# Kernel optimization log

Hardware: AMD Instinct MI355X
Metric: run time of the kernel (lower is better)

Reference implementation:

```python
import jax, jax.numpy as jnp
import numpy as np
from jax import lax

NUM_QUBITS = 4
NUM_LAYERS = 2
EPS = 1e-5  # BatchNorm eps; eval mode with running_mean=0, running_var=1


def _cnot_ring_matrix():
    # CNOT(0,1); CNOT(1,2); CNOT(2,3); CNOT(3,0) as one 16x16 permutation.
    # PennyLane convention: wire 0 is the most-significant bit of the basis index.
    M = np.zeros((16, 16), dtype=np.complex64)
    for b in range(16):
        bb = b
        for cw, tw in [(0, 1), (1, 2), (2, 3), (3, 0)]:
            if (bb >> (3 - cw)) & 1:
                bb ^= 1 << (3 - tw)
        M[bb, b] = 1.0
    return M

CNOT_RING = jnp.asarray(_cnot_ring_matrix())
# ZSIGNS[w, b] = <b|Z_w|b> = +/-1
ZSIGNS = jnp.asarray(np.array([[1.0 - 2.0 * ((b >> (3 - w)) & 1) for b in range(16)]
                               for w in range(NUM_QUBITS)], dtype=np.float32))


def conv_bn_relu(x, w, b, gamma, beta):
    # Conv2d(k=3, pad=1) + BatchNorm2d (eval: mean=0, var=1) + ReLU, NCHW
    x = lax.conv_general_dilated(x, w, (1, 1), ((1, 1), (1, 1)),
                                 dimension_numbers=('NCHW', 'OIHW', 'NCHW'))
    x = x + b[None, :, None, None]
    x = gamma[None, :, None, None] * x * (1.0 / np.sqrt(1.0 + EPS)) + beta[None, :, None, None]
    return jax.nn.relu(x)


def maxpool2(x):
    return lax.reduce_window(x, -jnp.inf, lax.max, (1, 1, 2, 2), (1, 1, 2, 2), 'VALID')


def avgpool2(x):
    return lax.reduce_window(x, 0.0, lax.add, (1, 1, 2, 2), (1, 1, 2, 2), 'VALID') * 0.25


def quantum_layer(x, weights):
    # x: [B, 16] softmax outputs. Amplitude-encode (abs + L2 normalize), then
    # BasicEntanglerLayers (RX rotations + CNOT ring) x NUM_LAYERS, then <Z_i>.
    psi = jnp.abs(x)
    psi = psi / jnp.linalg.norm(psi, axis=1, keepdims=True)
    psi = psi.astype(jnp.complex64)  # [B, 16] batched statevectors
    for l in range(NUM_LAYERS):
        c = jnp.cos(weights[l] * 0.5).astype(jnp.complex64)
        s = jnp.sin(weights[l] * 0.5).astype(jnp.complex64)
        U = jnp.ones((1, 1), dtype=jnp.complex64)
        for q in range(NUM_QUBITS):
            g = jnp.stack([jnp.stack([c[q], -1j * s[q]]),
                           jnp.stack([-1j * s[q], c[q]])])  # RX(theta_q)
            U = jnp.kron(U, g)
        U = CNOT_RING @ U  # rotations first, then entangling ring
        psi = psi @ U.T    # batched apply: [B,16] x [16,16]
    probs = jnp.real(psi * jnp.conj(psi))  # [B, 16]
    return probs @ ZSIGNS.T                # [B, 4] Pauli-Z expvals


def setup_inputs() -> dict:
    key = jax.random.key(0)
    ks = jax.random.split(key, 16)
    B = 1024
    f32 = jnp.float32

    def w(k, shape, fan_in):
        return jax.random.normal(k, shape, dtype=f32) * np.float32(1.0 / np.sqrt(fan_in))

    inp = {
        'x': jax.random.normal(ks[0], (B, 3, 32, 32), dtype=f32),
        'conv1_w': w(ks[1], (32, 3, 3, 3), 3 * 9), 'conv1_b': jnp.zeros((32,), f32),
        'bn1_g': jnp.ones((32,), f32), 'bn1_b': jnp.zeros((32,), f32),
        'conv2_w': w(ks[2], (64, 32, 3, 3), 32 * 9), 'conv2_b': jnp.zeros((64,), f32),
        'bn2_g': jnp.ones((64,), f32), 'bn2_b': jnp.zeros((64,), f32),
        'conv3_w': w(ks[3], (128, 64, 3, 3), 64 * 9), 'conv3_b': jnp.zeros((128,), f32),
        'bn3_g': jnp.ones((128,), f32), 'bn3_b': jnp.zeros((128,), f32),
        'fr1_w': w(ks[4], (512, 2048), 2048), 'fr1_b': jnp.zeros((512,), f32),
        'fr2_w': w(ks[5], (16, 512), 512), 'fr2_b': jnp.zeros((16,), f32),
        'q_weights': jax.random.uniform(ks[6], (NUM_LAYERS, NUM_QUBITS), dtype=f32,
                                        minval=0.0, maxval=2.0 * np.pi),
        'h1_w': w(ks[7], (128, 4), 4), 'h1_b': jnp.zeros((128,), f32),
        'bnh_g': jnp.ones((128,), f32), 'bnh_b': jnp.zeros((128,), f32),
        'h2_w': w(ks[8], (100, 128), 128), 'h2_b': jnp.zeros((100,), f32),
    }
    return inp


def reference(x, conv1_w, conv1_b, bn1_g, bn1_b, conv2_w, conv2_b, bn2_g, bn2_b,
              conv3_w, conv3_b, bn3_g, bn3_b, fr1_w, fr1_b, fr2_w, fr2_b,
              q_weights, h1_w, h1_b, bnh_g, bnh_b, h2_w, h2_b):
    # classical_net (CIFAR100 branch)
    h = conv_bn_relu(x, conv1_w, conv1_b, bn1_g, bn1_b)
    h = maxpool2(h)                                   # [B,32,16,16]
    h = conv_bn_relu(h, conv2_w, conv2_b, bn2_g, bn2_b)
    h = maxpool2(h)                                   # [B,64,8,8]
    h = conv_bn_relu(h, conv3_w, conv3_b, bn3_g, bn3_b)  # [B,128,8,8]
    h = avgpool2(h)                                   # AdaptiveAvgPool2d((4,4)): 8->4
    h = h.reshape(h.shape[0], -1)                     # [B, 2048]
    # feature_reducer
    h = jax.nn.relu(h @ fr1_w.T + fr1_b)
    f = jax.nn.softmax(h @ fr2_w.T + fr2_b, axis=1)   # [B, 16]
    # quantum layer (batched 4-qubit statevector sim)
    q = quantum_layer(f, q_weights)                   # [B, 4]
    # head (BN eval-mode, Dropout inactive)
    y = q @ h1_w.T + h1_b
    y = bnh_g * y * (1.0 / np.sqrt(1.0 + EPS)) + bnh_b
    y = jax.nn.relu(y)
    return y @ h2_w.T + h2_b                          # [B, 100]
```

## Files before the change

kernel.cpp:

```cpp
#include <hip/hip_runtime.h>
#include <math.h>

#define NB 1024
static constexpr float BN_INV = 0.99999500003749975f;

typedef __attribute__((ext_vector_type(8))) short short8;
typedef __attribute__((ext_vector_type(4))) float f32x4;

__device__ inline short f2bf(float f) {
  union { float f; unsigned u; } v;
  v.f = f;
  unsigned u = v.u;
  u += 0x7fff + ((u >> 16) & 1);
  return (short)(u >> 16);
}

__global__ void k_prepack(const float* __restrict__ c2w, const float* __restrict__ c2b,
                          const float* __restrict__ g2, const float* __restrict__ be2,
                          const float* __restrict__ c3w, const float* __restrict__ c3b,
                          const float* __restrict__ g3, const float* __restrict__ be3,
                          const float* __restrict__ fr1w,
                          short* __restrict__ wp2, short* __restrict__ wp3,
                          float* __restrict__ scsh, short* __restrict__ wfr1) {
  int i = blockIdx.x * 256 + threadIdx.x;
  int stride = gridDim.x * 256;
  for (int e = i; e < 18432; e += stride) {
    int j = e & 7, lane = (e >> 3) & 63, ct = (e >> 9) & 3, off = e >> 11;
    int co = ct * 16 + (lane & 15), ci = (lane >> 4) * 8 + j;
    wp2[e] = f2bf(c2w[(co * 32 + ci) * 9 + off]);
  }
  for (int e = i; e < 73728; e += stride) {
    int j = e & 7, lane = (e >> 3) & 63, ct = (e >> 9) & 7, oh = e >> 12;
    int half = oh & 1, off = oh >> 1;
    int co = ct * 16 + (lane & 15), ci = half * 32 + (lane >> 4) * 8 + j;
    wp3[e] = f2bf(c3w[(co * 64 + ci) * 9 + off]);
  }
  for (int e = i; e < 524288; e += stride) {
    float2 f = ((const float2*)fr1w)[e];
    unsigned lo = (unsigned)(unsigned short)f2bf(f.x);
    unsigned hi = (unsigned)(unsigned short)f2bf(f.y);
    ((unsigned*)wfr1)[e] = (hi << 16) | lo;
  }
  if (i < 64) {
    float sc = g2[i] * BN_INV;
    scsh[i] = sc;
    scsh[64 + i] = sc * c2b[i] + be2[i];
  } else if (i < 192) {
    int c = i - 64;
    float sc = g3[c] * BN_INV;
    scsh[128 + c] = sc;
    scsh[256 + c] = sc * c3b[c] + be3[c];
  }
}

__global__ __launch_bounds__(256) void k_conv1(
    const float* __restrict__ x, const float* __restrict__ w,
    const float* __restrict__ bias, const float* __restrict__ g,
    const float* __restrict__ be, short* __restrict__ out) {
  __shared__ float tile[3 * 34 * 34];
  const int b = blockIdx.x;
  const int tid = threadIdx.x;
  const float* xb = x + b * 3 * 32 * 32;
  for (int i = tid; i < 3 * 34 * 34; i += 256) {
    int c = i / 1156;
    int rem = i - c * 1156;
    int r = rem / 34;
    int col = rem - r * 34;
    int iy = r - 1, ix = col - 1;
    float v = 0.f;
    if (iy >= 0 && iy < 32 && ix >= 0 && ix < 32)
      v = xb[(c * 32 + iy) * 32 + ix];
    tile[i] = v;
  }
  __syncthreads();
  const int tx = tid & 15, ty = tid >> 4;
  float win[3][4][4];
#pragma unroll
  for (int c = 0; c < 3; ++c)
#pragma unroll
    for (int r = 0; r < 4; ++r)
#pragma unroll
      for (int cc = 0; cc < 4; ++cc)
        win[c][r][cc] = tile[c * 1156 + (2 * ty + r) * 34 + 2 * tx + cc];

  for (int co = 0; co < 32; ++co) {
    const float* wp = w + co * 27;
    float a00 = 0.f, a01 = 0.f, a10 = 0.f, a11 = 0.f;
#pragma unroll
    for (int c = 0; c < 3; ++c)
#pragma unroll
      for (int ky = 0; ky < 3; ++ky)
#pragma unroll
        for (int kx = 0; kx < 3; ++kx) {
          float wv = wp[c * 9 + ky * 3 + kx];
          a00 = fmaf(win[c][ky][kx], wv, a00);
          a01 = fmaf(win[c][ky][kx + 1], wv, a01);
          a10 = fmaf(win[c][ky + 1][kx], wv, a10);
          a11 = fmaf(win[c][ky + 1][kx + 1], wv, a11);
        }
    float gg = g[co] * BN_INV, bt = be[co], bs = bias[co];
    float v0 = fmaxf(fmaf(gg, a00 + bs, bt), 0.f);
    float v1 = fmaxf(fmaf(gg, a01 + bs, bt), 0.f);
    float v2 = fmaxf(fmaf(gg, a10 + bs, bt), 0.f);
    float v3 = fmaxf(fmaf(gg, a11 + bs, bt), 0.f);
    float m = fmaxf(fmaxf(v0, v1), fmaxf(v2, v3));
    out[((b * 32 + co) * 16 + ty) * 16 + tx] = f2bf(m);
  }
}

__global__ __launch_bounds__(256) void k_conv2m(
    const short* __restrict__ in ,
    const short* __restrict__ wp2, const float* __restrict__ scsh,
    short* __restrict__ out2 ) {
  __shared__ __align__(16) short inT[18 * 18 * 40];
  const int b = blockIdx.x;
  const int tid = threadIdx.x;
  const int w = tid >> 6, lane = tid & 63, q = lane >> 4, n = lane & 15;

  for (int i = tid; i < 18 * 18 * 40 / 2; i += 256) ((int*)inT)[i] = 0;
  __syncthreads();
  const short* ib = in + (size_t)b * 8192;
  for (int i = tid; i < 8192; i += 256) {
    int ci = i >> 8, y = (i >> 4) & 15, x = i & 15;
    inT[((y + 1) * 18 + (x + 1)) * 40 + ci] = ib[i];
  }
  __syncthreads();

  const short8* wv = (const short8*)wp2;
  f32x4 acc[4][4];
#pragma unroll
  for (int t = 0; t < 4; ++t)
#pragma unroll
    for (int ct = 0; ct < 4; ++ct) acc[t][ct] = (f32x4)0.f;

#pragma unroll
  for (int off = 0; off < 9; ++off) {
    const int ky = off / 3, kx = off % 3;
    short8 a[4];
#pragma unroll
    for (int ct = 0; ct < 4; ++ct) a[ct] = wv[(off * 4 + ct) * 64 + lane];
#pragma unroll
    for (int t = 0; t < 4; ++t) {
      int y = 4 * w + t;
      short8 bf = *(const short8*)&inT[((y + ky) * 18 + (n + kx)) * 40 + q * 8];
#pragma unroll
      for (int ct = 0; ct < 4; ++ct)
        acc[t][ct] =
            __builtin_amdgcn_mfma_f32_16x16x32_bf16(a[ct], bf, acc[t][ct], 0, 0, 0);
    }
  }

  const float* sc2 = scsh;
  const float* sh2 = scsh + 64;
#pragma unroll
  for (int ct = 0; ct < 4; ++ct) {
    float vm[4][4];
#pragma unroll
    for (int t = 0; t < 4; ++t)
#pragma unroll
      for (int r = 0; r < 4; ++r) {
        int co = ct * 16 + q * 4 + r;
        float v = fmaf(sc2[co], acc[t][ct][r], sh2[co]);
        v = fmaxf(v, 0.f);
        vm[t][r] = fmaxf(v, __shfl_xor(v, 1));
      }
#pragma unroll
    for (int pp = 0; pp < 2; ++pp)
#pragma unroll
      for (int r = 0; r < 4; ++r) {
        float m = fmaxf(vm[2 * pp][r], vm[2 * pp + 1][r]);
        if ((n & 1) == 0) {
          int co = ct * 16 + q * 4 + r;
          out2[((size_t)b * 64 + co) * 64 + (2 * w + pp) * 8 + (n >> 1)] = f2bf(m);
        }
      }
  }
}

__global__ __launch_bounds__(256) void k_conv3m(
    const short* __restrict__ in ,
    const short* __restrict__ wp3, const float* __restrict__ scsh,
    short* __restrict__ out3 ) {
  __shared__ __align__(16) short inT3[10 * 10 * 72];
  const int b = blockIdx.x;
  const int tid = threadIdx.x;
  const int w = tid >> 6, lane = tid & 63, q = lane >> 4, n = lane & 15;

  for (int i = tid; i < 10 * 10 * 72 / 2; i += 256) ((int*)inT3)[i] = 0;
  __syncthreads();
  const short* ib = in + (size_t)b * 4096;
  for (int i = tid; i < 4096; i += 256) {
    int ci = i >> 6, y = (i >> 3) & 7, x = i & 7;
    inT3[((y + 1) * 10 + (x + 1)) * 72 + ci] = ib[i];
  }
  __syncthreads();

  const short8* wv = (const short8*)wp3;
  f32x4 acc[4][2];
#pragma unroll
  for (int c = 0; c < 4; ++c)
#pragma unroll
    for (int tt = 0; tt < 2; ++tt) acc[c][tt] = (f32x4)0.f;

  const int ct0 = (w >> 1) * 4;
  const int t0 = (w & 1) * 2;
#pragma unroll
  for (int off = 0; off < 9; ++off) {
    const int ky = off / 3, kx = off % 3;
#pragma unroll
    for (int half = 0; half < 2; ++half) {
      short8 a[4];
#pragma unroll
      for (int c = 0; c < 4; ++c)
        a[c] = wv[((off * 2 + half) * 8 + ct0 + c) * 64 + lane];
#pragma unroll
      for (int tt = 0; tt < 2; ++tt) {
        int y = 2 * (t0 + tt) + (n >> 3), x = n & 7;
        short8 bf = *(const short8*)&inT3[((y + ky) * 10 + (x + kx)) * 72 +
                                          half * 32 + q * 8];
#pragma unroll
        for (int c = 0; c < 4; ++c)
          acc[c][tt] =
              __builtin_amdgcn_mfma_f32_16x16x32_bf16(a[c], bf, acc[c][tt], 0, 0, 0);
      }
    }
  }

  const float* sc3 = scsh + 128;
  const float* sh3 = scsh + 256;
#pragma unroll
  for (int c = 0; c < 4; ++c) {
    int ct = ct0 + c;
#pragma unroll
    for (int tt = 0; tt < 2; ++tt) {
      int t = t0 + tt;
#pragma unroll
      for (int r = 0; r < 4; ++r) {
        int co = ct * 16 + q * 4 + r;
        float v = fmaf(sc3[co], acc[c][tt][r], sh3[co]);
        v = fmaxf(v, 0.f);
        float s = v + __shfl_xor(v, 1);
        s += __shfl_xor(s, 8);
        if ((n & 9) == 0)
          out3[(size_t)b * 2048 + co * 16 + t * 4 + (n >> 1)] = f2bf(s * 0.25f);
      }
    }
  }
}

__global__ __launch_bounds__(256) void k_fr1m(
    const short* __restrict__ A, const short* __restrict__ W,
    const float* __restrict__ bias, float* __restrict__ C) {
  __shared__ __align__(16) short As[32 * 72];
  __shared__ __align__(16) short Bs[32 * 72];
  const int m0 = blockIdx.x * 32;
  const int n0 = blockIdx.y * 32;
  const int tid = threadIdx.x;
  const int w = tid >> 6, lane = tid & 63, q = lane >> 4, n = lane & 15;
  const int mt = w >> 1, nt = w & 1;
  const int srow = tid >> 3, sc = tid & 7;

  f32x4 acc = (f32x4)0.f;
  const short* Ab = A + (size_t)(m0 + srow) * 2048 + sc * 8;
  const short* Wb = W + (size_t)(n0 + srow) * 2048 + sc * 8;

  for (int k0 = 0; k0 < 2048; k0 += 64) {
    short8 av = *(const short8*)(Ab + k0);
    short8 bv = *(const short8*)(Wb + k0);
    __syncthreads();
    *(short8*)&As[srow * 72 + sc * 8] = av;
    *(short8*)&Bs[srow * 72 + sc * 8] = bv;
    __syncthreads();
#pragma unroll
    for (int kk = 0; kk < 2; ++kk) {
      short8 bfrag = *(const short8*)&Bs[(nt * 16 + n) * 72 + kk * 32 + q * 8];
      short8 afrag = *(const short8*)&As[(mt * 16 + n) * 72 + kk * 32 + q * 8];
      acc = __builtin_amdgcn_mfma_f32_16x16x32_bf16(afrag, bfrag, acc, 0, 0, 0);
    }
  }
#pragma unroll
  for (int r = 0; r < 4; ++r) {
    int m = m0 + mt * 16 + q * 4 + r;
    int nn = n0 + nt * 16 + n;
    C[(size_t)m * 512 + nn] = fmaxf(acc[r] + bias[nn], 0.f);
  }
}

__global__ __launch_bounds__(64) void k_tail(
    const float* __restrict__ H, const float* __restrict__ W2,
    const float* __restrict__ b2, const float* __restrict__ qw,
    const float* __restrict__ h1w, const float* __restrict__ h1b,
    const float* __restrict__ bg, const float* __restrict__ bb,
    const float* __restrict__ h2w, const float* __restrict__ h2b,
    float* __restrict__ out) {
  __shared__ float hbuf[512];
  __shared__ float ybuf[128];
  const int b = blockIdx.x;
  const int lane = threadIdx.x;
  const float* hrow = H + b * 512;
  *(float4*)&hbuf[lane * 4] = *(const float4*)&hrow[lane * 4];
  *(float4*)&hbuf[256 + lane * 4] = *(const float4*)&hrow[256 + lane * 4];
  __syncthreads();

  const int j = lane & 15;
  const int grpk = lane >> 4;
  float partial = 0.f;
  const float* wrow = W2 + j * 512 + grpk * 128;
  const float* hb = hbuf + grpk * 128;
#pragma unroll
  for (int k = 0; k < 128; k += 4) {
    float4 wv = *(const float4*)&wrow[k];
    partial = fmaf(wv.x, hb[k + 0], partial);
    partial = fmaf(wv.y, hb[k + 1], partial);
    partial = fmaf(wv.z, hb[k + 2], partial);
    partial = fmaf(wv.w, hb[k + 3], partial);
  }
  partial += __shfl_xor(partial, 16);
  partial += __shfl_xor(partial, 32);
  float logit = partial + b2[j];

  float m = logit;
#pragma unroll
  for (int d = 1; d < 16; d <<= 1) m = fmaxf(m, __shfl_xor(m, d));
  float e = expf(logit - m);
  float s = e;
#pragma unroll
  for (int d = 1; d < 16; d <<= 1) s += __shfl_xor(s, d);
  float p = e / s;

  float n2 = p * p;
#pragma unroll
  for (int d = 1; d < 16; d <<= 1) n2 += __shfl_xor(n2, d);
  float amp = p / sqrtf(n2);
  float re = amp, im = 0.f;

#pragma unroll
  for (int l = 0; l < 2; ++l) {
#pragma unroll
    for (int q = 0; q < 4; ++q) {
      float th = qw[l * 4 + q] * 0.5f;
      float c = cosf(th), sn = sinf(th);
      int mask = 1 << (3 - q);
      float pre = __shfl_xor(re, mask);
      float pim = __shfl_xor(im, mask);
      float nre = fmaf(c, re, sn * pim);
      float nim = fmaf(c, im, -sn * pre);
      re = nre;
      im = nim;
    }
    int src = j;
    if (src & 1) src ^= 8;
    if (src & 2) src ^= 1;
    if (src & 4) src ^= 2;
    if (src & 8) src ^= 4;
    int srclane = (lane & 48) | src;
    re = __shfl(re, srclane);
    im = __shfl(im, srclane);
  }

  float prob = re * re + im * im;
  float qv[4];
#pragma unroll
  for (int w = 0; w < 4; ++w) {
    float sgn = ((j >> (3 - w)) & 1) ? -1.f : 1.f;
    float cwv = prob * sgn;
    cwv += __shfl_xor(cwv, 1);
    cwv += __shfl_xor(cwv, 2);
    cwv += __shfl_xor(cwv, 4);
    cwv += __shfl_xor(cwv, 8);
    qv[w] = cwv;
  }

#pragma unroll
  for (int t = 0; t < 2; ++t) {
    int jj = lane + 64 * t;
    float4 hw = *(const float4*)&h1w[jj * 4];
    float y = h1b[jj];
    y = fmaf(hw.x, qv[0], y);
    y = fmaf(hw.y, qv[1], y);
    y = fmaf(hw.z, qv[2], y);
    y = fmaf(hw.w, qv[3], y);
    y = fmaf(bg[jj] * BN_INV, y, bb[jj]);
    ybuf[jj] = fmaxf(y, 0.f);
  }
  __syncthreads();

#pragma unroll
  for (int t = 0; t < 2; ++t) {
    int k = lane + 64 * t;
    if (k < 100) {
      const float* wr = h2w + k * 128;
      float o = h2b[k];
#pragma unroll
      for (int jj = 0; jj < 128; jj += 4) {
        float4 wv = *(const float4*)&wr[jj];
        o = fmaf(wv.x, ybuf[jj + 0], o);
        o = fmaf(wv.y, ybuf[jj + 1], o);
        o = fmaf(wv.z, ybuf[jj + 2], o);
        o = fmaf(wv.w, ybuf[jj + 3], o);
      }
      out[b * 100 + k] = o;
    }
  }
}

extern "C" void kernel_launch(void* const* d_in, const int* in_sizes, int n_in,
                              void* d_out, int out_size, void* d_ws,
                              size_t ws_size, hipStream_t stream) {
  const float* x = (const float*)d_in[0];
  const float* c1w = (const float*)d_in[1];
  const float* c1b = (const float*)d_in[2];
  const float* g1 = (const float*)d_in[3];
  const float* be1 = (const float*)d_in[4];
  const float* c2w = (const float*)d_in[5];
  const float* c2b = (const float*)d_in[6];
  const float* g2 = (const float*)d_in[7];
  const float* be2 = (const float*)d_in[8];
  const float* c3w = (const float*)d_in[9];
  const float* c3b = (const float*)d_in[10];
  const float* g3 = (const float*)d_in[11];
  const float* be3 = (const float*)d_in[12];
  const float* fr1w = (const float*)d_in[13];
  const float* fr1b = (const float*)d_in[14];
  const float* fr2w = (const float*)d_in[15];
  const float* fr2b = (const float*)d_in[16];
  const float* qwts = (const float*)d_in[17];
  const float* h1w = (const float*)d_in[18];
  const float* h1b = (const float*)d_in[19];
  const float* bhg = (const float*)d_in[20];
  const float* bhb = (const float*)d_in[21];
  const float* h2w = (const float*)d_in[22];
  const float* h2b = (const float*)d_in[23];
  float* out = (float*)d_out;

  float* ws = (float*)d_ws;
  short* out1bf = (short*)ws;
  short* out2bf = (short*)(ws + 4194304);
  short* out3bf = (short*)(ws + 6291456);
  float* h1 = ws + 7340032;
  short* wfr1 = (short*)(ws + 7864320);
  short* wp2 = (short*)(ws + 8388608);
  short* wp3 = (short*)(ws + 8397824);
  float* scsh = ws + 8434688;

  k_prepack<<<96, 256, 0, stream>>>(c2w, c2b, g2, be2, c3w, c3b, g3, be3, fr1w,
                                    wp2, wp3, scsh, wfr1);
  k_conv1<<<NB, 256, 0, stream>>>(x, c1w, c1b, g1, be1, out1bf);
  k_conv2m<<<NB, 256, 0, stream>>>(out1bf, wp2, scsh, out2bf);
  k_conv3m<<<NB, 256, 0, stream>>>(out2bf, wp3, scsh, out3bf);
  k_fr1m<<<dim3(32, 16), 256, 0, stream>>>(out3bf, wfr1, fr1b, h1);
  k_tail<<<NB, 64, 0, stream>>>(h1, fr2w, fr2b, qwts, h1w, h1b, bhg, bhb, h2w,
                                h2b, out);
}
```

Measured before the change: 200.5 us.

## Fuse conv1, conv2 and conv3 into one per-image kernel using shared memory

Merges the three convolution stages into a single kernel per image. Intermediate activations stay in LDS, so the bf16 writes and reads of the conv1 and conv2 outputs through global memory are gone, and two launches are removed. The fr1 weight bf16 conversion moves out of the prepack kernel into 128 extra blocks of the fused kernel. The cost is a larger LDS footprint per block (about 40 KB, shared between overlapping buffers) and longer, more register-heavy blocks, which could lower occupancy.

```diff
diff --git a/kernel.cpp b/kernel.cpp
--- a/kernel.cpp
+++ b/kernel.cpp
@@ -19,9 +19,8 @@
                           const float* __restrict__ g2, const float* __restrict__ be2,
                           const float* __restrict__ c3w, const float* __restrict__ c3b,
                           const float* __restrict__ g3, const float* __restrict__ be3,
-                          const float* __restrict__ fr1w,
                           short* __restrict__ wp2, short* __restrict__ wp3,
-                          float* __restrict__ scsh, short* __restrict__ wfr1) {
+                          float* __restrict__ scsh) {
   int i = blockIdx.x * 256 + threadIdx.x;
   int stride = gridDim.x * 256;
   for (int e = i; e < 18432; e += stride) {
@@ -34,12 +33,6 @@
     int half = oh & 1, off = oh >> 1;
     int co = ct * 16 + (lane & 15), ci = half * 32 + (lane >> 4) * 8 + j;
     wp3[e] = f2bf(c3w[(co * 64 + ci) * 9 + off]);
-  }
-  for (int e = i; e < 524288; e += stride) {
-    float2 f = ((const float2*)fr1w)[e];
-    unsigned lo = (unsigned)(unsigned short)f2bf(f.x);
-    unsigned hi = (unsigned)(unsigned short)f2bf(f.y);
-    ((unsigned*)wfr1)[e] = (hi << 16) | lo;
   }
   if (i < 64) {
     float sc = g2[i] * BN_INV;
@@ -53,14 +46,36 @@
   }
 }
 
-__global__ __launch_bounds__(256) void k_conv1(
-    const float* __restrict__ x, const float* __restrict__ w,
-    const float* __restrict__ bias, const float* __restrict__ g,
-    const float* __restrict__ be, short* __restrict__ out) {
-  __shared__ float tile[3 * 34 * 34];
-  const int b = blockIdx.x;
+__global__ __launch_bounds__(256) void k_convfused(
+    const float* __restrict__ x, const float* __restrict__ w1,
+    const float* __restrict__ b1, const float* __restrict__ g1,
+    const float* __restrict__ be1, const short* __restrict__ wp2,
+    const short* __restrict__ wp3, const float* __restrict__ scsh,
+    const float* __restrict__ fr1w, short* __restrict__ wfr1,
+    short* __restrict__ out3 ) {
+  __shared__ __align__(16) char smem[40320];
   const int tid = threadIdx.x;
+  const int bx = blockIdx.x;
+
+  if (bx >= NB) {
+    int i = (bx - NB) * 256 + tid;
+    for (int e = i; e < 524288; e += 128 * 256) {
+      float2 f = ((const float2*)fr1w)[e];
+      unsigned lo = (unsigned)(unsigned short)f2bf(f.x);
+      unsigned hi = (unsigned)(unsigned short)f2bf(f.y);
+      ((unsigned*)wfr1)[e] = (hi << 16) | lo;
+    }
+    return;
+  }
+
+  short* inT = (short*)smem;
+  float* tile = (float*)(smem + 25920);
+  short* inT3 = (short*)(smem + 25920);
+
+  const int b = bx;
+
   const float* xb = x + b * 3 * 32 * 32;
+  for (int i = tid; i < 6480; i += 256) ((int*)inT)[i] = 0;
   for (int i = tid; i < 3 * 34 * 34; i += 256) {
     int c = i / 1156;
     int rem = i - c * 1156;
@@ -73,176 +88,162 @@
     tile[i] = v;
   }
   __syncthreads();
-  const int tx = tid & 15, ty = tid >> 4;
-  float win[3][4][4];
-#pragma unroll
-  for (int c = 0; c < 3; ++c)
-#pragma unroll
-    for (int r = 0; r < 4; ++r)
-#pragma unroll
-      for (int cc = 0; cc < 4; ++cc)
-        win[c][r][cc] = tile[c * 1156 + (2 * ty + r) * 34 + 2 * tx + cc];
-
-  for (int co = 0; co < 32; ++co) {
-    const float* wp = w + co * 27;
-    float a00 = 0.f, a01 = 0.f, a10 = 0.f, a11 = 0.f;
+
+  {
+    const int tx = tid & 15, ty = tid >> 4;
+    float win[3][4][4];
 #pragma unroll
     for (int c = 0; c < 3; ++c)
 #pragma unroll
-      for (int ky = 0; ky < 3; ++ky)
-#pragma unroll
-        for (int kx = 0; kx < 3; ++kx) {
-          float wv = wp[c * 9 + ky * 3 + kx];
-          a00 = fmaf(win[c][ky][kx], wv, a00);
-          a01 = fmaf(win[c][ky][kx + 1], wv, a01);
-          a10 = fmaf(win[c][ky + 1][kx], wv, a10);
-          a11 = fmaf(win[c][ky + 1][kx + 1], wv, a11);
+      for (int r = 0; r < 4; ++r)
+#pragma unroll
+        for (int cc = 0; cc < 4; ++cc)
+          win[c][r][cc] = tile[c * 1156 + (2 * ty + r) * 34 + 2 * tx + cc];
+
+    short cv[32];
+#pragma unroll
+    for (int co = 0; co < 32; ++co) {
+      const float* wp = w1 + co * 27;
+      float a00 = 0.f, a01 = 0.f, a10 = 0.f, a11 = 0.f;
+#pragma unroll
+      for (int c = 0; c < 3; ++c)
+#pragma unroll
+        for (int ky = 0; ky < 3; ++ky)
+#pragma unroll
+          for (int kx = 0; kx < 3; ++kx) {
+            float wv = wp[c * 9 + ky * 3 + kx];
+            a00 = fmaf(win[c][ky][kx], wv, a00);
+            a01 = fmaf(win[c][ky][kx + 1], wv, a01);
+            a10 = fmaf(win[c][ky + 1][kx], wv, a10);
+            a11 = fmaf(win[c][ky + 1][kx + 1], wv, a11);
+          }
+      float gg = g1[co] * BN_INV, bt = be1[co], bs = b1[co];
+      float v0 = fmaxf(fmaf(gg, a00 + bs, bt), 0.f);
+      float v1 = fmaxf(fmaf(gg, a01 + bs, bt), 0.f);
+      float v2 = fmaxf(fmaf(gg, a10 + bs, bt), 0.f);
+      float v3 = fmaxf(fmaf(gg, a11 + bs, bt), 0.f);
+      cv[co] = f2bf(fmaxf(fmaxf(v0, v1), fmaxf(v2, v3)));
+    }
+    short8* dst = (short8*)&inT[((ty + 1) * 18 + (tx + 1)) * 40];
+#pragma unroll
+    for (int k = 0; k < 4; ++k) {
+      short8 v;
+#pragma unroll
+      for (int j = 0; j < 8; ++j) v[j] = cv[k * 8 + j];
+      dst[k] = v;
+    }
+  }
+  __syncthreads();
+
+  for (int i = tid; i < 3600; i += 256) ((int*)inT3)[i] = 0;
+  __syncthreads();
+
+  const int wid = tid >> 6, lane = tid & 63, q = lane >> 4, n = lane & 15;
+
+  {
+    const short8* wv = (const short8*)wp2;
+    f32x4 acc[4][4];
+#pragma unroll
+    for (int t = 0; t < 4; ++t)
+#pragma unroll
+      for (int ct = 0; ct < 4; ++ct) acc[t][ct] = (f32x4)0.f;
+
+#pragma unroll
+    for (int off = 0; off < 9; ++off) {
+      const int ky = off / 3, kx = off % 3;
+      short8 a[4];
+#pragma unroll
+      for (int ct = 0; ct < 4; ++ct) a[ct] = wv[(off * 4 + ct) * 64 + lane];
+#pragma unroll
+      for (int t = 0; t < 4; ++t) {
+        int y = 4 * wid + t;
+        short8 bf = *(const short8*)&inT[((y + ky) * 18 + (n + kx)) * 40 + q * 8];
+#pragma unroll
+        for (int ct = 0; ct < 4; ++ct)
+          acc[t][ct] = __builtin_amdgcn_mfma_f32_16x16x32_bf16(a[ct], bf,
+                                                               acc[t][ct], 0, 0, 0);
+      }
+    }
+
+    const float* sc2 = scsh;
+    const float* sh2 = scsh + 64;
+#pragma unroll
+    for (int ct = 0; ct < 4; ++ct) {
+      float vm[4][4];
+#pragma unroll
+      for (int t = 0; t < 4; ++t)
+#pragma unroll
+        for (int r = 0; r < 4; ++r) {
+          int co = ct * 16 + q * 4 + r;
+          float v = fmaf(sc2[co], acc[t][ct][r], sh2[co]);
+          v = fmaxf(v, 0.f);
+          vm[t][r] = fmaxf(v, __shfl_xor(v, 1));
         }
-    float gg = g[co] * BN_INV, bt = be[co], bs = bias[co];
-    float v0 = fmaxf(fmaf(gg, a00 + bs, bt), 0.f);
-    float v1 = fmaxf(fmaf(gg, a01 + bs, bt), 0.f);
-    float v2 = fmaxf(fmaf(gg, a10 + bs, bt), 0.f);
-    float v3 = fmaxf(fmaf(gg, a11 + bs, bt), 0.f);
-    float m = fmaxf(fmaxf(v0, v1), fmaxf(v2, v3));
-    out[((b * 32 + co) * 16 + ty) * 16 + tx] = f2bf(m);
-  }
-}
-
-__global__ __launch_bounds__(256) void k_conv2m(
-    const short* __restrict__ in ,
-    const short* __restrict__ wp2, const float* __restrict__ scsh,
-    short* __restrict__ out2 ) {
-  __shared__ __align__(16) short inT[18 * 18 * 40];
-  const int b = blockIdx.x;
-  const int tid = threadIdx.x;
-  const int w = tid >> 6, lane = tid & 63, q = lane >> 4, n = lane & 15;
-
-  for (int i = tid; i < 18 * 18 * 40 / 2; i += 256) ((int*)inT)[i] = 0;
-  __syncthreads();
-  const short* ib = in + (size_t)b * 8192;
-  for (int i = tid; i < 8192; i += 256) {
-    int ci = i >> 8, y = (i >> 4) & 15, x = i & 15;
-    inT[((y + 1) * 18 + (x + 1)) * 40 + ci] = ib[i];
-  }
-  __syncthreads();
-
-  const short8* wv = (const short8*)wp2;
-  f32x4 acc[4][4];
-#pragma unroll
-  for (int t = 0; t < 4; ++t)
-#pragma unroll
-    for (int ct = 0; ct < 4; ++ct) acc[t][ct] = (f32x4)0.f;
-
-#pragma unroll
-  for (int off = 0; off < 9; ++off) {
-    const int ky = off / 3, kx = off % 3;
-    short8 a[4];
-#pragma unroll
-    for (int ct = 0; ct < 4; ++ct) a[ct] = wv[(off * 4 + ct) * 64 + lane];
-#pragma unroll
-    for (int t = 0; t < 4; ++t) {
-      int y = 4 * w + t;
-      short8 bf = *(const short8*)&inT[((y + ky) * 18 + (n + kx)) * 40 + q * 8];
-#pragma unroll
-      for (int ct = 0; ct < 4; ++ct)
-        acc[t][ct] =
-            __builtin_amdgcn_mfma_f32_16x16x32_bf16(a[ct], bf, acc[t][ct], 0, 0, 0);
-    }
-  }
-
-  const float* sc2 = scsh;
-  const float* sh2 = scsh + 64;
-#pragma unroll
-  for (int ct = 0; ct < 4; ++ct) {
-    float vm[4][4];
-#pragma unroll
-    for (int t = 0; t < 4; ++t)
-#pragma unroll
-      for (int r = 0; r < 4; ++r) {
-        int co = ct * 16 + q * 4 + r;
-        float v = fmaf(sc2[co], acc[t][ct][r], sh2[co]);
-        v = fmaxf(v, 0.f);
-        vm[t][r] = fmaxf(v, __shfl_xor(v, 1));
-      }
-#pragma unroll
-    for (int pp = 0; pp < 2; ++pp)
-#pragma unroll
-      for (int r = 0; r < 4; ++r) {
-        float m = fmaxf(vm[2 * pp][r], vm[2 * pp + 1][r]);
-        if ((n & 1) == 0) {
-          int co = ct * 16 + q * 4 + r;
-          out2[((size_t)b * 64 + co) * 64 + (2 * w + pp) * 8 + (n >> 1)] = f2bf(m);
+#pragma unroll
+      for (int pp = 0; pp < 2; ++pp)
+#pragma unroll
+        for (int r = 0; r < 4; ++r) {
+          float m = fmaxf(vm[2 * pp][r], vm[2 * pp + 1][r]);
+          if ((n & 1) == 0) {
+            int co = ct * 16 + q * 4 + r;
+            int y2 = 2 * wid + pp, x2 = n >> 1;
+            inT3[((y2 + 1) * 10 + (x2 + 1)) * 72 + co] = f2bf(m);
+          }
+        }
+    }
+  }
+  __syncthreads();
+
+  {
+    const short8* wv = (const short8*)wp3;
+    f32x4 acc[4][2];
+#pragma unroll
+    for (int c = 0; c < 4; ++c)
+#pragma unroll
+      for (int tt = 0; tt < 2; ++tt) acc[c][tt] = (f32x4)0.f;
+
+    const int ct0 = (wid >> 1) * 4;
+    const int t0 = (wid & 1) * 2;
+#pragma unroll
+    for (int off = 0; off < 9; ++off) {
+      const int ky = off / 3, kx = off % 3;
+#pragma unroll
+      for (int half = 0; half < 2; ++half) {
+        short8 a[4];
+#pragma unroll
+        for (int c = 0; c < 4; ++c)
+          a[c] = wv[((off * 2 + half) * 8 + ct0 + c) * 64 + lane];
+#pragma unroll
+        for (int tt = 0; tt < 2; ++tt) {
+          int y = 2 * (t0 + tt) + (n >> 3), xx = n & 7;
+          short8 bf = *(const short8*)&inT3[((y + ky) * 10 + (xx + kx)) * 72 +
+                                            half * 32 + q * 8];
+#pragma unroll
+          for (int c = 0; c < 4; ++c)
+            acc[c][tt] = __builtin_amdgcn_mfma_f32_16x16x32_bf16(a[c], bf,
+                                                                 acc[c][tt], 0, 0, 0);
         }
       }
-  }
-}
-
-__global__ __launch_bounds__(256) void k_conv3m(
-    const short* __restrict__ in ,
-    const short* __restrict__ wp3, const float* __restrict__ scsh,
-    short* __restrict__ out3 ) {
-  __shared__ __align__(16) short inT3[10 * 10 * 72];
-  const int b = blockIdx.x;
-  const int tid = threadIdx.x;
-  const int w = tid >> 6, lane = tid & 63, q = lane >> 4, n = lane & 15;
-
-  for (int i = tid; i < 10 * 10 * 72 / 2; i += 256) ((int*)inT3)[i] = 0;
-  __syncthreads();
-  const short* ib = in + (size_t)b * 4096;
-  for (int i = tid; i < 4096; i += 256) {
-    int ci = i >> 6, y = (i >> 3) & 7, x = i & 7;
-    inT3[((y + 1) * 10 + (x + 1)) * 72 + ci] = ib[i];
-  }
-  __syncthreads();
-
-  const short8* wv = (const short8*)wp3;
-  f32x4 acc[4][2];
-#pragma unroll
-  for (int c = 0; c < 4; ++c)
-#pragma unroll
-    for (int tt = 0; tt < 2; ++tt) acc[c][tt] = (f32x4)0.f;
-
-  const int ct0 = (w >> 1) * 4;
-  const int t0 = (w & 1) * 2;
-#pragma unroll
-  for (int off = 0; off < 9; ++off) {
-    const int ky = off / 3, kx = off % 3;
-#pragma unroll
-    for (int half = 0; half < 2; ++half) {
-      short8 a[4];
-#pragma unroll
-      for (int c = 0; c < 4; ++c)
-        a[c] = wv[((off * 2 + half) * 8 + ct0 + c) * 64 + lane];
+    }
+
+    const float* sc3 = scsh + 128;
+    const float* sh3 = scsh + 256;
+#pragma unroll
+    for (int c = 0; c < 4; ++c) {
+      int ct = ct0 + c;
 #pragma unroll
       for (int tt = 0; tt < 2; ++tt) {
-        int y = 2 * (t0 + tt) + (n >> 3), x = n & 7;
-        short8 bf = *(const short8*)&inT3[((y + ky) * 10 + (x + kx)) * 72 +
-                                          half * 32 + q * 8];
-#pragma unroll
-        for (int c = 0; c < 4; ++c)
-          acc[c][tt] =
-              __builtin_amdgcn_mfma_f32_16x16x32_bf16(a[c], bf, acc[c][tt], 0, 0, 0);
-      }
-    }
-  }
-
-  const float* sc3 = scsh + 128;
-  const float* sh3 = scsh + 256;
-#pragma unroll
-  for (int c = 0; c < 4; ++c) {
-    int ct = ct0 + c;
-#pragma unroll
-    for (int tt = 0; tt < 2; ++tt) {
-      int t = t0 + tt;
-#pragma unroll
-      for (int r = 0; r < 4; ++r) {
-        int co = ct * 16 + q * 4 + r;
-        float v = fmaf(sc3[co], acc[c][tt][r], sh3[co]);
-        v = fmaxf(v, 0.f);
-        float s = v + __shfl_xor(v, 1);
-        s += __shfl_xor(s, 8);
-        if ((n & 9) == 0)
-          out3[(size_t)b * 2048 + co * 16 + t * 4 + (n >> 1)] = f2bf(s * 0.25f);
+        int t = t0 + tt;
+#pragma unroll
+        for (int r = 0; r < 4; ++r) {
+          int co = ct * 16 + q * 4 + r;
+          float v = fmaf(sc3[co], acc[c][tt][r], sh3[co]);
+          v = fmaxf(v, 0.f);
+          float s = v + __shfl_xor(v, 1);
+          s += __shfl_xor(s, 8);
+          if ((n & 9) == 0)
+            out3[(size_t)b * 2048 + co * 16 + t * 4 + (n >> 1)] = f2bf(s * 0.25f);
+        }
       }
     }
   }
@@ -434,20 +435,17 @@
   float* out = (float*)d_out;
 
   float* ws = (float*)d_ws;
-  short* out1bf = (short*)ws;
-  short* out2bf = (short*)(ws + 4194304);
-  short* out3bf = (short*)(ws + 6291456);
-  float* h1 = ws + 7340032;
-  short* wfr1 = (short*)(ws + 7864320);
-  short* wp2 = (short*)(ws + 8388608);
-  short* wp3 = (short*)(ws + 8397824);
-  float* scsh = ws + 8434688;
-
-  k_prepack<<<96, 256, 0, stream>>>(c2w, c2b, g2, be2, c3w, c3b, g3, be3, fr1w,
-                                    wp2, wp3, scsh, wfr1);
-  k_conv1<<<NB, 256, 0, stream>>>(x, c1w, c1b, g1, be1, out1bf);
-  k_conv2m<<<NB, 256, 0, stream>>>(out1bf, wp2, scsh, out2bf);
-  k_conv3m<<<NB, 256, 0, stream>>>(out2bf, wp3, scsh, out3bf);
+  short* out3bf = (short*)ws;
+  float* h1 = ws + 1048576;
+  short* wfr1 = (short*)(ws + 1572864);
+  short* wp2 = (short*)(ws + 2097152);
+  short* wp3 = (short*)(ws + 2106368);
+  float* scsh = ws + 2143232;
+
+  k_prepack<<<96, 256, 0, stream>>>(c2w, c2b, g2, be2, c3w, c3b, g3, be3,
+                                    wp2, wp3, scsh);
+  k_convfused<<<NB + 128, 256, 0, stream>>>(x, c1w, c1b, g1, be1, wp2, wp3,
+                                            scsh, fr1w, wfr1, out3bf);
   k_fr1m<<<dim3(32, 16), 256, 0, stream>>>(out3bf, wfr1, fr1b, h1);
   k_tail<<<NB, 64, 0, stream>>>(h1, fr2w, fr2b, qwts, h1w, h1b, bhg, bhb, h2w,
                                 h2b, out);
```

Result: slower. 207.2 us (+3.3%).
